# Kernel optimization log

Measured on AMD Instinct MI355X. Metric: run time of the kernel, lower is better.

## Reference

```python
import jax, jax.numpy as jnp
import numpy as np

N_HEAD = 16
D_HEAD = 64
N_GROUPS = 4
D_EMBED = 1024
ROPE_N = 32
B, T = 2, 2048


def apply_rope(x, cos, sin):
    # x: (..., T, ROPE_N); cos/sin: (T, ROPE_N) broadcast over leading dims
    h = x.shape[-1]
    x1, x2 = x[..., : h // 2], x[..., h // 2 :]
    rotated = jnp.concatenate((-x2, x1), axis=-1)
    return (x * cos + rotated * sin).astype(x.dtype)


def setup_inputs() -> dict:
    key = jax.random.key(0)
    k1, k2, k3, k4, k5 = jax.random.split(key, 5)
    return {
        "x": jax.random.normal(k1, (B, T, D_EMBED), dtype=jnp.float32),
        "cos": jax.random.uniform(k2, (T, ROPE_N), dtype=jnp.float32),
        "sin": jax.random.uniform(k3, (T, ROPE_N), dtype=jnp.float32),
        "mask": jnp.ones((B, T), dtype=bool),  # unused by the original forward (passes None to SDPA)
        "Wqkv": jax.random.normal(k4, (D_EMBED, (N_HEAD + 2 * N_GROUPS) * D_HEAD), dtype=jnp.float32) * 0.02,
        "Wout": jax.random.normal(k5, (N_HEAD * D_HEAD, D_EMBED), dtype=jnp.float32) * 0.02,
    }


def reference(x, cos, sin, mask, Wqkv, Wout):
    Bv, Tv, _ = x.shape
    q_per_kv = N_HEAD // N_GROUPS  # 4
    total_qkv = q_per_kv + 2       # 6

    qkv = jnp.einsum("btc,cf->btf", x, Wqkv)  # (B, T, 1536)
    qkv = qkv.reshape(Bv, Tv, N_GROUPS, total_qkv, D_HEAD)
    qkv = jnp.transpose(qkv, (0, 2, 3, 1, 4))  # (B, G, total_qkv, T, d)

    q = qkv[:, :, :q_per_kv]           # (B, G, q_per_kv, T, d)
    k = qkv[:, :, q_per_kv : q_per_kv + 1]  # (B, G, 1, T, d)
    v = qkv[:, :, q_per_kv + 1 :]           # (B, G, 1, T, d)

    # GQA expand (1 < groups < heads)
    k = jnp.broadcast_to(k, (Bv, N_GROUPS, q_per_kv, Tv, D_HEAD))
    v = jnp.broadcast_to(v, (Bv, N_GROUPS, q_per_kv, Tv, D_HEAD))

    q = q.reshape(Bv, N_HEAD, Tv, D_HEAD)
    k = k.reshape(Bv, N_HEAD, Tv, D_HEAD)
    v = v.reshape(Bv, N_HEAD, Tv, D_HEAD)

    # partial RoPE on the first ROPE_N dims of each head
    q = jnp.concatenate((apply_rope(q[..., :ROPE_N], cos, sin), q[..., ROPE_N:]), axis=-1)
    k = jnp.concatenate((apply_rope(k[..., :ROPE_N], cos, sin), k[..., ROPE_N:]), axis=-1)

    scale = 1.0 / np.sqrt(D_HEAD).astype(np.float32)
    scores = jnp.einsum("bhtd,bhsd->bhts", q, k) * scale
    attn = jax.nn.softmax(scores, axis=-1)
    y = jnp.einsum("bhts,bhsd->bhtd", attn, v)   # (B, H, T, d)
    y = jnp.transpose(y, (0, 2, 1, 3)).reshape(Bv, Tv, N_HEAD * D_HEAD)
    return jnp.einsum("btf,fc->btc", y, Wout)
```

## Files before the change

kernel.cpp:

```cpp
#include <hip/hip_runtime.h>
#include <hip/hip_bf16.h>
#include <math.h>

#define BATCH   2
#define TSEQ    2048
#define DEMBED  1024
#define NHEAD   16
#define DHEAD   64
#define NGROUP  4
#define ROPEN   32
#define FQKV    1536
#define MROWS   (BATCH*TSEQ)

typedef __attribute__((ext_vector_type(8))) short short8;
typedef __attribute__((ext_vector_type(4))) float floatx4;

__device__ __forceinline__ void split_pack8(const float* f, uint4& h4, uint4& l4) {
    uint u[8], lu[8];
    #pragma unroll
    for (int j = 0; j < 8; ++j) {
        u[j] = __float_as_uint(f[j]);
        float lf = f[j] - __uint_as_float(u[j] & 0xffff0000u);
        lu[j] = __float_as_uint(lf);
    }
    h4.x = __builtin_amdgcn_perm(u[1], u[0], 0x07060302u);
    h4.y = __builtin_amdgcn_perm(u[3], u[2], 0x07060302u);
    h4.z = __builtin_amdgcn_perm(u[5], u[4], 0x07060302u);
    h4.w = __builtin_amdgcn_perm(u[7], u[6], 0x07060302u);
    l4.x = __builtin_amdgcn_perm(lu[1], lu[0], 0x07060302u);
    l4.y = __builtin_amdgcn_perm(lu[3], lu[2], 0x07060302u);
    l4.z = __builtin_amdgcn_perm(lu[5], lu[4], 0x07060302u);
    l4.w = __builtin_amdgcn_perm(lu[7], lu[6], 0x07060302u);
}

__device__ __forceinline__ void rtn_pack8(const float* f, uint4& h4) {
    uint t[8];
    #pragma unroll
    for (int j = 0; j < 8; ++j)
        t[j] = __float_as_uint(f[j]) + 0x8000u;
    h4.x = __builtin_amdgcn_perm(t[1], t[0], 0x07060302u);
    h4.y = __builtin_amdgcn_perm(t[3], t[2], 0x07060302u);
    h4.z = __builtin_amdgcn_perm(t[5], t[4], 0x07060302u);
    h4.w = __builtin_amdgcn_perm(t[7], t[6], 0x07060302u);
}

__device__ __forceinline__ uint pk_bf16x2(float f0, float f1) {
    uint u0 = __float_as_uint(f0) + 0x8000u;
    uint u1 = __float_as_uint(f1) + 0x8000u;
    return __builtin_amdgcn_perm(u1, u0, 0x07060302u);
}

__device__ __forceinline__ float fast_exp2(float x) {
    float r;
    asm("v_exp_f32 %0, %1" : "=v"(r) : "v"(x));
    return r;
}

__device__ __forceinline__ void lds_async16(void* lds, const void* gp) {
    __builtin_amdgcn_global_load_lds(
        (const __attribute__((address_space(1))) unsigned int*)gp,
        (__attribute__((address_space(3))) unsigned int*)lds,
        16, 0, 0);
}


__global__ __launch_bounds__(256) void conv_xy(const float* __restrict__ in,
                                               char* __restrict__ img) {
    const int tid = threadIdx.x;
    const int c   = blockIdx.x & 15;
    const int mt  = blockIdx.x >> 4;
    const int r    = tid >> 1;
    const int half = tid & 1;

    const float* src = in + (size_t)(mt*128 + r)*1024 + c*64 + half*32;
    float f[32];
    #pragma unroll
    for (int u = 0; u < 8; ++u)
        *(float4*)(f + 4*u) = *(const float4*)(src + 4*u);

    char* tile = img + ((size_t)(mt*16 + c)) * 32768;
    #pragma unroll
    for (int cc = 0; cc < 4; ++cc) {
        uint4 h4, l4;
        split_pack8(f + cc*8, h4, l4);
        int j    = half*4 + cc;
        int phys = j ^ (r & 7);
        *(uint4*)(tile + r*128 + phys*16)         = h4;
        *(uint4*)(tile + 16384 + r*128 + phys*16) = l4;
    }
}

__global__ __launch_bounds__(256) void conv_w(const float* __restrict__ W,
                                              int N,
                                              char* __restrict__ img) {
    __shared__ float Lf[64][132];
    const int tid = threadIdx.x;
    const int c   = blockIdx.x;
    const int nt  = blockIdx.y;

    {
        const int kk = tid >> 2;
        const int nc = (tid & 3) * 32;
        const float* src = W + (size_t)(c*64 + kk)*N + nt*128 + nc;
        #pragma unroll
        for (int u = 0; u < 8; ++u)
            *(float4*)(&Lf[kk][nc + 4*u]) = *(const float4*)(src + 4*u);
    }
    __syncthreads();

    char* tile = img + ((size_t)(nt*16 + c)) * 32768;
    #pragma unroll
    for (int rep = 0; rep < 4; ++rep) {
        int idx = rep*256 + tid;
        int n = idx & 127;
        int j = idx >> 7;
        float v[8];
        #pragma unroll
        for (int i = 0; i < 8; ++i) v[i] = Lf[j*8 + i][n];
        uint4 h4, l4;
        split_pack8(v, h4, l4);
        int phys = j ^ (n & 7);
        *(uint4*)(tile + n*128 + phys*16)         = h4;
        *(uint4*)(tile + 16384 + n*128 + phys*16) = l4;
    }
}

struct GemmAcc { floatx4 a[4][4]; };

__device__ __forceinline__ void gemm_mfma_core(const char* __restrict__ Aimg,
                                               const char* __restrict__ Bimg,
                                               char* smem, int mt, int nt,
                                               int tid, GemmAcc& G) {
    const int wv = tid >> 6;
    const int wm = wv & 1, wn = wv >> 1;
    const int lane = tid & 63;
    const int qd = lane >> 4, cl = lane & 15;
    const int wslot = (tid & 192) * 16;

    #pragma unroll
    for (int tm = 0; tm < 4; ++tm)
        #pragma unroll
        for (int tn = 0; tn < 4; ++tn)
            G.a[tm][tn] = (floatx4){0.f, 0.f, 0.f, 0.f};

    for (int c = 0; c < 16; ++c) {
        __syncthreads();
        {
            const uint4* gA = (const uint4*)(Aimg + ((size_t)(mt*16 + c)) * 32768) + tid;
            const uint4* gB = (const uint4*)(Bimg + ((size_t)(nt*16 + c)) * 32768) + tid;
            #pragma unroll
            for (int j = 0; j < 8; ++j) {
                lds_async16(smem + j*4096 + wslot,         gA + j*256);
                lds_async16(smem + 32768 + j*4096 + wslot, gB + j*256);
            }
        }
        __syncthreads();

        #pragma unroll
        for (int s = 0; s < 2; ++s) {
            const int phys = ((s*4 + qd) ^ (cl & 7)) * 16;
            short8 ah[4], al[4], bh[4], bl[4];
            #pragma unroll
            for (int tt = 0; tt < 4; ++tt) {
                const int rA = wm*64 + 16*tt + cl;
                ah[tt] = *(const short8*)(smem + rA*128 + phys);
                al[tt] = *(const short8*)(smem + 16384 + rA*128 + phys);
                const int rB = wn*64 + 16*tt + cl;
                bh[tt] = *(const short8*)(smem + 32768 + rB*128 + phys);
                bl[tt] = *(const short8*)(smem + 49152 + rB*128 + phys);
            }
            #pragma unroll
            for (int tm = 0; tm < 4; ++tm)
                #pragma unroll
                for (int tn = 0; tn < 4; ++tn) {
                    G.a[tm][tn] = __builtin_amdgcn_mfma_f32_16x16x32_bf16(ah[tm], bh[tn], G.a[tm][tn], 0, 0, 0);
                    G.a[tm][tn] = __builtin_amdgcn_mfma_f32_16x16x32_bf16(al[tm], bh[tn], G.a[tm][tn], 0, 0, 0);
                    G.a[tm][tn] = __builtin_amdgcn_mfma_f32_16x16x32_bf16(ah[tm], bl[tn], G.a[tm][tn], 0, 0, 0);
                }
        }
    }
}

__global__ __launch_bounds__(256, 2) void gemm_qkv_mfma(const char* __restrict__ Aimg,
                                                        const char* __restrict__ Bimg,
                                                        const float* __restrict__ cosp,
                                                        const float* __restrict__ sinp,
                                                        float* __restrict__ Qf,
                                                        ushort* __restrict__ Kimg,
                                                        ushort* __restrict__ Vimg) {
    __shared__ __align__(16) char smem[68608];
    const int tid = threadIdx.x;
    const int nt = blockIdx.x, mt = blockIdx.y;

    GemmAcc G;
    gemm_mfma_core(Aimg, Bimg, smem, mt, nt, tid, G);

    const int wv = tid >> 6;
    const int wm = wv & 1, wn = wv >> 1;
    const int lane = tid & 63;
    const int qd = lane >> 4, cl = lane & 15;

    const int slice = nt*2 + wn;
    const int g  = slice / 6;
    const int jj = slice % 6;
    const int b  = mt >> 4;

    if (jj != 5) {
        #pragma unroll
        for (int tm = 0; tm < 4; ++tm)
            #pragma unroll
            for (int r = 0; r < 4; ++r) {
                int m = mt*128 + wm*64 + 16*tm + 4*qd + r;
                int t = m & 2047;
                float c1 = cosp[t*ROPEN + cl],      s1 = sinp[t*ROPEN + cl];
                float c2 = cosp[t*ROPEN + 16 + cl], s2 = sinp[t*ROPEN + 16 + cl];
                float x1 = G.a[tm][0][r], x2 = G.a[tm][1][r];
                G.a[tm][0][r] = x1*c1 - x2*s1;
                G.a[tm][1][r] = x2*c2 + x1*s2;
            }
    }

    if (jj < 4) {
        #pragma unroll
        for (int tm = 0; tm < 4; ++tm)
            #pragma unroll
            for (int tn = 0; tn < 4; ++tn)
                #pragma unroll
                for (int r = 0; r < 4; ++r) {
                    int m = mt*128 + wm*64 + 16*tm + 4*qd + r;
                    Qf[(size_t)m*1024 + (g*4 + jj)*64 + 16*tn + cl] = G.a[tm][tn][r];
                }
    } else {
        float* Lw = (float*)(smem + wv*17152);
        __syncthreads();
        #pragma unroll
        for (int tm = 0; tm < 4; ++tm)
            #pragma unroll
            for (int tn = 0; tn < 4; ++tn)
                #pragma unroll
                for (int r = 0; r < 4; ++r)
                    Lw[(16*tm + 4*qd + r)*67 + 16*tn + cl] = G.a[tm][tn][r];
        __syncthreads();

        const int cloc = (mt & 15)*2 + wm;
        ushort* img = ((jj == 4) ? Kimg : Vimg)
                      + (size_t)(b*4 + g)*262144 + (size_t)cloc*8192;
        if (jj == 4) {
            const int rr = lane;
            float f[8];
            #pragma unroll
            for (int ch = 0; ch < 8; ++ch) {
                *(float4*)f       = *(const float4*)(&Lw[rr*67 + ch*8]);
                *(float4*)(f + 4) = *(const float4*)(&Lw[rr*67 + ch*8 + 4]);
                uint4 h4, l4;
                split_pack8(f, h4, l4);
                int phys = ch ^ (rr & 7);
                *(uint4*)(img + rr*64 + phys*8)        = h4;
                *(uint4*)(img + 4096 + rr*64 + phys*8) = l4;
            }
        } else {
            const int d = lane;
            float f[8];
            #pragma unroll
            for (int ch = 0; ch < 8; ++ch) {
                const int kb = 32*(ch >> 2) + 4*(ch & 3);
                #pragma unroll
                for (int i = 0; i < 4; ++i) f[i]     = Lw[(kb + i)*67 + d];
                #pragma unroll
                for (int i = 0; i < 4; ++i) f[4 + i] = Lw[(kb + 16 + i)*67 + d];
                uint4 h4;
                rtn_pack8(f, h4);
                int phys = ch ^ (d & 7);
                *(uint4*)(img + d*64 + phys*8) = h4;
            }
        }
    }
}

__global__ __launch_bounds__(256, 2) void gemm_out_mfma(const char* __restrict__ Aimg,
                                                        const char* __restrict__ Bimg,
                                                        float* __restrict__ C) {
    __shared__ __align__(16) char smem[49152];
    const int tid = threadIdx.x;
    const int nt = blockIdx.x, mt = blockIdx.y;

    const int wv = tid >> 6;
    const int wm = wv & 1, wn = wv >> 1;
    const int lane = tid & 63;
    const int qd = lane >> 4, cl = lane & 15;
    const int wslot = (tid & 192) * 16;

    floatx4 acc[2][4];
    #pragma unroll
    for (int tm = 0; tm < 2; ++tm)
        #pragma unroll
        for (int tn = 0; tn < 4; ++tn)
            acc[tm][tn] = (floatx4){0.f, 0.f, 0.f, 0.f};

    for (int c = 0; c < 16; ++c) {
        __syncthreads();
        {
            const char* sA = Aimg + ((size_t)((mt >> 1)*16 + c))*32768
                                  + (mt & 1)*8192 + (size_t)tid*16;
            const char* sB = Bimg + ((size_t)(nt*16 + c))*32768 + (size_t)tid*16;
            lds_async16(smem + wslot,          sA);
            lds_async16(smem + 4096  + wslot,  sA + 4096);
            lds_async16(smem + 8192  + wslot,  sA + 16384);
            lds_async16(smem + 12288 + wslot,  sA + 16384 + 4096);
            #pragma unroll
            for (int j = 0; j < 4; ++j) {
                lds_async16(smem + 16384 + j*4096 + wslot, sB + j*4096);
                lds_async16(smem + 32768 + j*4096 + wslot, sB + 16384 + j*4096);
            }
        }
        __syncthreads();

        #pragma unroll
        for (int s = 0; s < 2; ++s) {
            const int phys = ((s*4 + qd) ^ (cl & 7)) * 16;
            short8 ah[2], al[2], bh[4], bl[4];
            #pragma unroll
            for (int tt = 0; tt < 2; ++tt) {
                const int rA = wm*32 + 16*tt + cl;
                ah[tt] = *(const short8*)(smem + rA*128 + phys);
                al[tt] = *(const short8*)(smem + 8192 + rA*128 + phys);
            }
            #pragma unroll
            for (int tt = 0; tt < 4; ++tt) {
                const int rB = wn*64 + 16*tt + cl;
                bh[tt] = *(const short8*)(smem + 16384 + rB*128 + phys);
                bl[tt] = *(const short8*)(smem + 32768 + rB*128 + phys);
            }
            #pragma unroll
            for (int tm = 0; tm < 2; ++tm)
                #pragma unroll
                for (int tn = 0; tn < 4; ++tn) {
                    acc[tm][tn] = __builtin_amdgcn_mfma_f32_16x16x32_bf16(ah[tm], bh[tn], acc[tm][tn], 0, 0, 0);
                    acc[tm][tn] = __builtin_amdgcn_mfma_f32_16x16x32_bf16(al[tm], bh[tn], acc[tm][tn], 0, 0, 0);
                    acc[tm][tn] = __builtin_amdgcn_mfma_f32_16x16x32_bf16(ah[tm], bl[tn], acc[tm][tn], 0, 0, 0);
                }
        }
    }

    #pragma unroll
    for (int tm = 0; tm < 2; ++tm)
        #pragma unroll
        for (int tn = 0; tn < 4; ++tn)
            #pragma unroll
            for (int r = 0; r < 4; ++r) {
                int m = mt*64 + wm*32 + 16*tm + 4*qd + r;
                int n = nt*128 + wn*64 + 16*tn + cl;
                C[(size_t)m*1024 + n] = acc[tm][tn][r];
            }
}

__global__ __launch_bounds__(512, 4) void attn14(const float* __restrict__ Qf,
                                                 const char* __restrict__ Kimg,
                                                 const char* __restrict__ Vimg,
                                                 char* __restrict__ Yimg) {
    __shared__ __align__(16) char smem[49152];

    const int tid  = threadIdx.x;
    const int wv8  = tid >> 6;
    const int grp  = wv8 >> 2;
    const int wq   = wv8 & 3;
    const int lane = tid & 63;
    const int qd   = lane >> 4;
    const int cl   = lane & 15;

    const int bg    = blockIdx.x & 7;
    const int inner = blockIdx.x >> 3;
    const int hj    = inner >> 5;
    const int qt    = inner & 31;
    const int b = bg >> 2, g = bg & 3;
    const int h = g*4 + hj;

    short8 qh[2], ql[2];
    {
        const float* qp = Qf + (size_t)(b*2048 + qt*64 + wq*16 + cl)*1024
                             + h*64 + 8*qd;
        #pragma unroll
        for (int s = 0; s < 2; ++s) {
            float f[8];
            *(float4*)f       = *(const float4*)(qp + 32*s);
            *(float4*)(f + 4) = *(const float4*)(qp + 32*s + 4);
            #pragma unroll
            for (int i = 0; i < 8; ++i) f[i] *= 0.125f * 1.44269504088896f;
            uint4 h4, l4;
            split_pack8(f, h4, l4);
            qh[s] = __builtin_bit_cast(short8, h4);
            ql[s] = __builtin_bit_cast(short8, l4);
        }
    }

    floatx4 accOT[4] = {};
    float lsum = 0.f;

    const char* Kg0 = Kimg + (size_t)bg*524288;
    const char* Vg0 = Vimg + (size_t)bg*524288;
    const int wslot = wv8 << 10;

    int voff[4];
    #pragma unroll
    for (int tt = 0; tt < 4; ++tt)
        voff[tt] = (16*tt + cl)*128 + (((4*grp + qd) ^ (cl & 7))*16);

    {
        const char* ksrc = Kg0 + (size_t)tid*16;
        lds_async16(smem + wslot,        ksrc);
        lds_async16(smem + 8192 + wslot, ksrc + 8192);
        lds_async16(smem + 32768 + wslot, Vg0 + (size_t)tid*16);
    }

    for (int c = 0; c < TSEQ/64; ++c) {
        __syncthreads();
        const int buf = c & 1;

        if (c + 1 < TSEQ/64) {
            const char* ksrc = Kg0 + (size_t)(c+1)*16384 + (size_t)tid*16;
            const char* vsrc = Vg0 + (size_t)(c+1)*16384 + (size_t)tid*16;
            lds_async16(smem + (1-buf)*16384 + wslot,        ksrc);
            lds_async16(smem + (1-buf)*16384 + 8192 + wslot, ksrc + 8192);
            lds_async16(smem + 32768 + (1-buf)*8192 + wslot, vsrc);
        }
        const char* Kl = smem + buf*16384;
        const char* Vl = smem + 32768 + buf*8192;

        floatx4 accST[2] = {};
        __builtin_amdgcn_s_setprio(1);
        #pragma unroll
        for (int s = 0; s < 2; ++s) {
            #pragma unroll
            for (int tt = 0; tt < 2; ++tt) {
                const int off = (32*grp + 16*tt + cl)*128
                              + (((4*s + qd) ^ (cl & 7))*16);
                short8 kh = *(const short8*)(Kl + off);
                short8 kl = *(const short8*)(Kl + 8192 + off);
                accST[tt] = __builtin_amdgcn_mfma_f32_16x16x32_bf16(kh, qh[s], accST[tt], 0, 0, 0);
                accST[tt] = __builtin_amdgcn_mfma_f32_16x16x32_bf16(kh, ql[s], accST[tt], 0, 0, 0);
                accST[tt] = __builtin_amdgcn_mfma_f32_16x16x32_bf16(kl, qh[s], accST[tt], 0, 0, 0);
            }
        }
        __builtin_amdgcn_s_setprio(0);

        float p[8];
        #pragma unroll
        for (int tt = 0; tt < 2; ++tt)
            #pragma unroll
            for (int r = 0; r < 4; ++r)
                p[4*tt + r] = fast_exp2(accST[tt][r]);
        lsum += ((p[0] + p[1]) + (p[2] + p[3]))
              + ((p[4] + p[5]) + (p[6] + p[7]));
        uint4 paw;
        paw.x = pk_bf16x2(p[0], p[1]);
        paw.y = pk_bf16x2(p[2], p[3]);
        paw.z = pk_bf16x2(p[4], p[5]);
        paw.w = pk_bf16x2(p[6], p[7]);
        short8 pa = __builtin_bit_cast(short8, paw);

        __builtin_amdgcn_s_setprio(1);
        #pragma unroll
        for (int tt = 0; tt < 4; ++tt) {
            short8 vh = *(const short8*)(Vl + voff[tt]);
            accOT[tt] = __builtin_amdgcn_mfma_f32_16x16x32_bf16(vh, pa, accOT[tt], 0, 0, 0);
        }
        __builtin_amdgcn_s_setprio(0);
    }

    __syncthreads();
    float* Pb = (float*)smem;
    if (grp == 1) {
        float* dst = Pb + (size_t)(wq*64 + lane)*17;
        #pragma unroll
        for (int tt = 0; tt < 4; ++tt)
            #pragma unroll
            for (int r = 0; r < 4; ++r)
                dst[4*tt + r] = accOT[tt][r];
        dst[16] = lsum;
    }
    __syncthreads();
    float* Lt = (float*)(smem + 17920);
    if (grp == 0) {
        const float* sp = Pb + (size_t)(wq*64 + lane)*17;
        #pragma unroll
        for (int tt = 0; tt < 4; ++tt)
            #pragma unroll
            for (int r = 0; r < 4; ++r)
                accOT[tt][r] += sp[4*tt + r];
        float l = lsum + sp[16];
        l += __shfl_xor(l, 16);
        l += __shfl_xor(l, 32);
        float inv = 1.0f / l;
        const int row = 16*wq + cl;
        #pragma unroll
        for (int tt = 0; tt < 4; ++tt)
            #pragma unroll
            for (int r = 0; r < 4; ++r)
                Lt[row*66 + 16*tt + 4*qd + r] = accOT[tt][r] * inv;
    }
    __syncthreads();
    {
        const int r0 = tid >> 3;
        const int qq = tid & 7;
        float f[8];
        #pragma unroll
        for (int u = 0; u < 4; ++u)
            *(float2*)(f + 2*u) = *(const float2*)(&Lt[r0*66 + qq*8 + 2*u]);
        const int R = (qt & 1)*64 + r0;
        char* tile = Yimg + (size_t)((b*16 + (qt >> 1))*16 + h) * 32768;
        uint4 h4, l4;
        split_pack8(f, h4, l4);
        int phys = qq ^ (R & 7);
        *(uint4*)(tile + R*128 + phys*16)         = h4;
        *(uint4*)(tile + 16384 + R*128 + phys*16) = l4;
    }
}

extern "C" void kernel_launch(void* const* d_in, const int* in_sizes, int n_in,
                              void* d_out, int out_size, void* d_ws, size_t ws_size,
                              hipStream_t stream) {
    const float* x    = (const float*)d_in[0];
    const float* cosp = (const float*)d_in[1];
    const float* sinp = (const float*)d_in[2];
    const float* Wqkv = (const float*)d_in[4];
    const float* Wout = (const float*)d_in[5];
    float* out = (float*)d_out;

    char* ws = (char*)d_ws;
    float*  Qf    = (float*)(ws);
    ushort* Kimg  = (ushort*)(ws + ((size_t)16<<20));
    ushort* Vimg  = (ushort*)(ws + ((size_t)20<<20));
    char*   Bo    = ws + ((size_t)24<<20);
    char*   Ximg  = ws + ((size_t)28<<20);
    char*   Bq    = ws + ((size_t)44<<20);
    char*   Yimg  = ws + ((size_t)28<<20);

    conv_xy<<<512, 256, 0, stream>>>(x, Ximg);
    conv_w<<<dim3(16, 12), 256, 0, stream>>>(Wqkv, FQKV, Bq);
    conv_w<<<dim3(16, 8), 256, 0, stream>>>(Wout, DEMBED, Bo);
    gemm_qkv_mfma<<<dim3(12, 32), 256, 0, stream>>>(Ximg, Bq, cosp, sinp,
                                                    Qf, Kimg, Vimg);
    attn14<<<1024, 512, 0, stream>>>(Qf, (const char*)Kimg, (const char*)Vimg,
                                     Yimg);
    gemm_out_mfma<<<dim3(8, 64), 256, 0, stream>>>(Yimg, Bo, out);
}
```

Measured before the change: 230.1 us.

## Process two query row-blocks per wave to reuse K/V tiles in attention

Each attention block now covers 128 query rows instead of 64, with every wave holding two 16-row query fragments that share each K and V fragment loaded from LDS. The grid halves to 512 blocks, so each K/V chunk is streamed from global memory and LDS half as often per query row. In exchange, register pressure rises (doubled accumulators and Q fragments) under launch bounds of 4, there are fewer blocks to fill the GPU, and the epilogue gains an extra barrier and reuses shared memory for the output staging.

```diff
diff --git a/kernel.cpp b/kernel.cpp
--- a/kernel.cpp
+++ b/kernel.cpp
@@ -354,7 +354,7 @@
             }
 }
 
-__global__ __launch_bounds__(512, 4) void attn14(const float* __restrict__ Qf,
+__global__ __launch_bounds__(512, 4) void attn15(const float* __restrict__ Qf,
                                                  const char* __restrict__ Kimg,
                                                  const char* __restrict__ Vimg,
                                                  char* __restrict__ Yimg) {
@@ -370,14 +370,15 @@
 
     const int bg    = blockIdx.x & 7;
     const int inner = blockIdx.x >> 3;
-    const int hj    = inner >> 5;
-    const int qt    = inner & 31;
+    const int hj    = inner >> 4;
+    const int qt    = inner & 15;
     const int b = bg >> 2, g = bg & 3;
     const int h = g*4 + hj;
 
-    short8 qh[2], ql[2];
-    {
-        const float* qp = Qf + (size_t)(b*2048 + qt*64 + wq*16 + cl)*1024
+    short8 qh[2][2], ql[2][2];
+    #pragma unroll
+    for (int rb = 0; rb < 2; ++rb) {
+        const float* qp = Qf + (size_t)(b*2048 + qt*128 + wq*32 + rb*16 + cl)*1024
                              + h*64 + 8*qd;
         #pragma unroll
         for (int s = 0; s < 2; ++s) {
@@ -388,13 +389,13 @@
             for (int i = 0; i < 8; ++i) f[i] *= 0.125f * 1.44269504088896f;
             uint4 h4, l4;
             split_pack8(f, h4, l4);
-            qh[s] = __builtin_bit_cast(short8, h4);
-            ql[s] = __builtin_bit_cast(short8, l4);
-        }
-    }
-
-    floatx4 accOT[4] = {};
-    float lsum = 0.f;
+            qh[rb][s] = __builtin_bit_cast(short8, h4);
+            ql[rb][s] = __builtin_bit_cast(short8, l4);
+        }
+    }
+
+    floatx4 accOT[2][4] = {};
+    float lsum[2] = {};
 
     const char* Kg0 = Kimg + (size_t)bg*524288;
     const char* Vg0 = Vimg + (size_t)bg*524288;
@@ -426,7 +427,7 @@
         const char* Kl = smem + buf*16384;
         const char* Vl = smem + 32768 + buf*8192;
 
-        floatx4 accST[2] = {};
+        floatx4 accST[2][2] = {};
         __builtin_amdgcn_s_setprio(1);
         #pragma unroll
         for (int s = 0; s < 2; ++s) {
@@ -436,33 +437,42 @@
                               + (((4*s + qd) ^ (cl & 7))*16);
                 short8 kh = *(const short8*)(Kl + off);
                 short8 kl = *(const short8*)(Kl + 8192 + off);
-                accST[tt] = __builtin_amdgcn_mfma_f32_16x16x32_bf16(kh, qh[s], accST[tt], 0, 0, 0);
-                accST[tt] = __builtin_amdgcn_mfma_f32_16x16x32_bf16(kh, ql[s], accST[tt], 0, 0, 0);
-                accST[tt] = __builtin_amdgcn_mfma_f32_16x16x32_bf16(kl, qh[s], accST[tt], 0, 0, 0);
+                #pragma unroll
+                for (int rb = 0; rb < 2; ++rb) {
+                    accST[rb][tt] = __builtin_amdgcn_mfma_f32_16x16x32_bf16(kh, qh[rb][s], accST[rb][tt], 0, 0, 0);
+                    accST[rb][tt] = __builtin_amdgcn_mfma_f32_16x16x32_bf16(kh, ql[rb][s], accST[rb][tt], 0, 0, 0);
+                    accST[rb][tt] = __builtin_amdgcn_mfma_f32_16x16x32_bf16(kl, qh[rb][s], accST[rb][tt], 0, 0, 0);
+                }
             }
         }
         __builtin_amdgcn_s_setprio(0);
 
-        float p[8];
-        #pragma unroll
-        for (int tt = 0; tt < 2; ++tt)
-            #pragma unroll
-            for (int r = 0; r < 4; ++r)
-                p[4*tt + r] = fast_exp2(accST[tt][r]);
-        lsum += ((p[0] + p[1]) + (p[2] + p[3]))
-              + ((p[4] + p[5]) + (p[6] + p[7]));
-        uint4 paw;
-        paw.x = pk_bf16x2(p[0], p[1]);
-        paw.y = pk_bf16x2(p[2], p[3]);
-        paw.z = pk_bf16x2(p[4], p[5]);
-        paw.w = pk_bf16x2(p[6], p[7]);
-        short8 pa = __builtin_bit_cast(short8, paw);
+        short8 pa[2];
+        #pragma unroll
+        for (int rb = 0; rb < 2; ++rb) {
+            float p[8];
+            #pragma unroll
+            for (int tt = 0; tt < 2; ++tt)
+                #pragma unroll
+                for (int r = 0; r < 4; ++r)
+                    p[4*tt + r] = fast_exp2(accST[rb][tt][r]);
+            lsum[rb] += ((p[0] + p[1]) + (p[2] + p[3]))
+                      + ((p[4] + p[5]) + (p[6] + p[7]));
+            uint4 paw;
+            paw.x = pk_bf16x2(p[0], p[1]);
+            paw.y = pk_bf16x2(p[2], p[3]);
+            paw.z = pk_bf16x2(p[4], p[5]);
+            paw.w = pk_bf16x2(p[6], p[7]);
+            pa[rb] = __builtin_bit_cast(short8, paw);
+        }
 
         __builtin_amdgcn_s_setprio(1);
         #pragma unroll
         for (int tt = 0; tt < 4; ++tt) {
             short8 vh = *(const short8*)(Vl + voff[tt]);
-            accOT[tt] = __builtin_amdgcn_mfma_f32_16x16x32_bf16(vh, pa, accOT[tt], 0, 0, 0);
+            #pragma unroll
+            for (int rb = 0; rb < 2; ++rb)
+                accOT[rb][tt] = __builtin_amdgcn_mfma_f32_16x16x32_bf16(vh, pa[rb], accOT[rb][tt], 0, 0, 0);
         }
         __builtin_amdgcn_s_setprio(0);
     }
@@ -470,49 +480,65 @@
     __syncthreads();
     float* Pb = (float*)smem;
     if (grp == 1) {
-        float* dst = Pb + (size_t)(wq*64 + lane)*17;
-        #pragma unroll
-        for (int tt = 0; tt < 4; ++tt)
-            #pragma unroll
-            for (int r = 0; r < 4; ++r)
-                dst[4*tt + r] = accOT[tt][r];
-        dst[16] = lsum;
+        #pragma unroll
+        for (int rb = 0; rb < 2; ++rb) {
+            float* dst = Pb + (size_t)(((wq*2 + rb)*64) + lane)*17;
+            #pragma unroll
+            for (int tt = 0; tt < 4; ++tt)
+                #pragma unroll
+                for (int r = 0; r < 4; ++r)
+                    dst[4*tt + r] = accOT[rb][tt][r];
+            dst[16] = lsum[rb];
+        }
     }
     __syncthreads();
-    float* Lt = (float*)(smem + 17920);
+    float inv[2] = {1.f, 1.f};
     if (grp == 0) {
-        const float* sp = Pb + (size_t)(wq*64 + lane)*17;
-        #pragma unroll
-        for (int tt = 0; tt < 4; ++tt)
-            #pragma unroll
-            for (int r = 0; r < 4; ++r)
-                accOT[tt][r] += sp[4*tt + r];
-        float l = lsum + sp[16];
-        l += __shfl_xor(l, 16);
-        l += __shfl_xor(l, 32);
-        float inv = 1.0f / l;
-        const int row = 16*wq + cl;
-        #pragma unroll
-        for (int tt = 0; tt < 4; ++tt)
-            #pragma unroll
-            for (int r = 0; r < 4; ++r)
-                Lt[row*66 + 16*tt + 4*qd + r] = accOT[tt][r] * inv;
+        #pragma unroll
+        for (int rb = 0; rb < 2; ++rb) {
+            const float* sp = Pb + (size_t)(((wq*2 + rb)*64) + lane)*17;
+            #pragma unroll
+            for (int tt = 0; tt < 4; ++tt)
+                #pragma unroll
+                for (int r = 0; r < 4; ++r)
+                    accOT[rb][tt][r] += sp[4*tt + r];
+            float l = lsum[rb] + sp[16];
+            l += __shfl_xor(l, 16);
+            l += __shfl_xor(l, 32);
+            inv[rb] = 1.0f / l;
+        }
+    }
+    __syncthreads();
+    float* Lt = (float*)smem;
+    if (grp == 0) {
+        #pragma unroll
+        for (int rb = 0; rb < 2; ++rb) {
+            const int row = wq*32 + rb*16 + cl;
+            #pragma unroll
+            for (int tt = 0; tt < 4; ++tt)
+                #pragma unroll
+                for (int r = 0; r < 4; ++r)
+                    Lt[row*66 + 16*tt + 4*qd + r] = accOT[rb][tt][r] * inv[rb];
+        }
     }
     __syncthreads();
     {
-        const int r0 = tid >> 3;
-        const int qq = tid & 7;
-        float f[8];
-        #pragma unroll
-        for (int u = 0; u < 4; ++u)
-            *(float2*)(f + 2*u) = *(const float2*)(&Lt[r0*66 + qq*8 + 2*u]);
-        const int R = (qt & 1)*64 + r0;
-        char* tile = Yimg + (size_t)((b*16 + (qt >> 1))*16 + h) * 32768;
-        uint4 h4, l4;
-        split_pack8(f, h4, l4);
-        int phys = qq ^ (R & 7);
-        *(uint4*)(tile + R*128 + phys*16)         = h4;
-        *(uint4*)(tile + 16384 + R*128 + phys*16) = l4;
+        char* tile = Yimg + (size_t)((b*16 + qt)*16 + h) * 32768;
+        #pragma unroll
+        for (int cc = 0; cc < 2; ++cc) {
+            const int idx = tid*2 + cc;
+            const int r0 = idx >> 3;
+            const int j  = idx & 7;
+            float f[8];
+            #pragma unroll
+            for (int u = 0; u < 4; ++u)
+                *(float2*)(f + 2*u) = *(const float2*)(&Lt[r0*66 + j*8 + 2*u]);
+            uint4 h4, l4;
+            split_pack8(f, h4, l4);
+            int phys = j ^ (r0 & 7);
+            *(uint4*)(tile + r0*128 + phys*16)         = h4;
+            *(uint4*)(tile + 16384 + r0*128 + phys*16) = l4;
+        }
     }
 }
 
@@ -540,7 +566,7 @@
     conv_w<<<dim3(16, 8), 256, 0, stream>>>(Wout, DEMBED, Bo);
     gemm_qkv_mfma<<<dim3(12, 32), 256, 0, stream>>>(Ximg, Bq, cosp, sinp,
                                                     Qf, Kimg, Vimg);
-    attn14<<<1024, 512, 0, stream>>>(Qf, (const char*)Kimg, (const char*)Vimg,
-                                     Yimg);
+    attn15<<<512, 512, 0, stream>>>(Qf, (const char*)Kimg, (const char*)Vimg,
+                                    Yimg);
     gemm_out_mfma<<<dim3(8, 64), 256, 0, stream>>>(Yimg, Bo, out);
 }
```

After: 224.2 us. -2.5%, faster.
